# Kernel optimization log

Hardware: AMD Instinct MI355X
Metric: run time of the kernel (lower is better)

The kernel has to match this reference:

```python
import jax, jax.numpy as jnp
import numpy as np

F_FIELDS = 39
VOCAB = 100000
EMB = 16
BATCH = 16384
H1, H2 = 32, 32


def setup_inputs() -> dict:
    key = jax.random.key(0)
    ks = jax.random.split(key, 10)
    Xi = jax.random.randint(ks[0], (BATCH, F_FIELDS, 1), 0, VOCAB, dtype=jnp.int64 if jax.config.jax_enable_x64 else jnp.int32).astype(jnp.int32)
    Xv = jax.random.uniform(ks[1], (BATCH, F_FIELDS), dtype=jnp.float32)
    # per-field embedding tables, stacked (all feature_sizes equal)
    emb1 = jax.random.normal(ks[2], (F_FIELDS, VOCAB, 1), dtype=jnp.float32)
    emb2 = jax.random.normal(ks[3], (F_FIELDS, VOCAB, EMB), dtype=jnp.float32)
    d_in = F_FIELDS * EMB
    W1 = jax.random.normal(ks[4], (d_in, H1), dtype=jnp.float32) / np.sqrt(d_in)
    b1 = jnp.zeros((H1,), dtype=jnp.float32)
    W2 = jax.random.normal(ks[5], (H1, H2), dtype=jnp.float32) / np.sqrt(H1)
    b2 = jnp.zeros((H2,), dtype=jnp.float32)
    bias = jax.random.normal(ks[6], (1,), dtype=jnp.float32)
    return {"Xi": Xi, "Xv": Xv, "emb1": emb1, "emb2": emb2,
            "W1": W1, "b1": b1, "W2": W2, "b2": b2, "bias": bias}


def reference(Xi, Xv, emb1, emb2, W1, b1, W2, b2, bias):
    B = Xi.shape[0]
    idx = Xi[:, :, 0]  # [B, F]
    # flatten per-field tables into one big table; offset indices by field
    off = idx + (jnp.arange(F_FIELDS, dtype=idx.dtype) * VOCAB)[None, :]  # [B, F]
    # first order: gather scalar per (b, f), scale by Xv
    first = emb1.reshape(F_FIELDS * VOCAB)[off] * Xv  # [B, F]
    # second order embeddings, scaled by Xv
    e2 = emb2.reshape(F_FIELDS * VOCAB, EMB)[off] * Xv[:, :, None]  # [B, F, E]
    s = jnp.sum(e2, axis=1)                      # [B, E]
    sq_sum = jnp.sum(e2 * e2, axis=1)            # [B, E]
    fm_second = 0.5 * (s * s - sq_sum)           # [B, E]
    # deep part on concatenated field embeddings
    deep_in = e2.reshape(B, F_FIELDS * EMB)
    h = jax.nn.relu(deep_in @ W1 + b1)
    h = jax.nn.relu(h @ W2 + b2)
    total = jnp.sum(first, axis=1) + jnp.sum(fm_second, axis=1) + jnp.sum(h, axis=1) + bias
    return total  # [B]
```

## Files before the change

### kernel.cpp

```cpp
#include <hip/hip_runtime.h>
#include <hip/hip_bf16.h>

#define F_FIELDS 39
#define VOCAB    100000
#define EMB      16
#define BATCH    16384
#define H1       32
#define H2       32
#define KSTEPS   20
#define KPW      10

typedef __bf16 bf16x8 __attribute__((ext_vector_type(8)));
typedef float  f32x4  __attribute__((ext_vector_type(4)));

__global__ __launch_bounds__(256) void swizzle_w1_kernel(const float* __restrict__ W1,
                                                         __bf16* __restrict__ ws)
{
    int fidx = blockIdx.x * 256 + threadIdx.x;
    if (fidx >= KSTEPS * 2 * 64) return;
    int lane = fidx & 63;
    int nh   = (fidx >> 6) & 1;
    int ks   = fidx >> 7;
    int k0   = ks * 32 + (lane >> 4) * 8;
    int n    = nh * 16 + (lane & 15);
    __bf16 vals[8];
    #pragma unroll
    for (int j = 0; j < 8; ++j) {
        int k = k0 + j;
        vals[j] = (k < F_FIELDS * EMB) ? (__bf16)W1[k * H1 + n] : (__bf16)0.0f;
    }
    *reinterpret_cast<bf16x8*>(&ws[fidx * 8]) = *reinterpret_cast<const bf16x8*>(vals);
}

__global__ __launch_bounds__(128, 2) void deepfm_main(
    const int*   __restrict__ Xi,  const float* __restrict__ Xv,
    const float* __restrict__ emb1,const float* __restrict__ emb2,
    const __bf16* __restrict__ wsW1,
    const float* __restrict__ b1,  const float* __restrict__ W2,
    const float* __restrict__ b2,  const float* __restrict__ bias,
    float* __restrict__ out)
{
    __shared__ float pacc[2][16][32];
    __shared__ float sbuf[2][16][16];
    __shared__ float qbuf[2][16];
    __shared__ float fbuf[2][16];
    __shared__ float W2s[H1 * H2];

    const int t    = threadIdx.x;
    const int h    = t >> 6;
    const int l    = t & 63;
    const int sloc = l & 15;
    const int q    = l >> 4;
    const int fpar = q >> 1;
    const int eoff = (q & 1) * 8;
    const int sample = blockIdx.x * 16 + sloc;
    const int xbase  = sample * F_FIELDS;

    #pragma unroll
    for (int i = 0; i < 2; ++i)
        reinterpret_cast<float4*>(W2s)[t + 128 * i] =
            reinterpret_cast<const float4*>(W2)[t + 128 * i];

    int   idxm[KPW]; float xvm[KPW];
    #pragma unroll
    for (int ks = 0; ks < KPW; ++ks) {
        int f = 4 * ks + 2 * h + fpar;
        bool v = (f < F_FIELDS);
        int fi = v ? f : 0;
        idxm[ks] = Xi[xbase + fi];
        xvm[ks]  = v ? Xv[xbase + fi] : 0.0f;
    }
    int idxf[5]; float xvf[5];
    #pragma unroll
    for (int i = 0; i < 5; ++i) {
        int f = h * 4 + q + 8 * i;
        bool v = (f < F_FIELDS);
        int fi = v ? f : 0;
        idxf[i] = Xi[xbase + fi];
        xvf[i]  = v ? Xv[xbase + fi] : 0.0f;
    }

    float4 g0[KPW], g1[KPW];
    bf16x8 fr0[KPW], fr1[KPW];
    const bf16x8* wsf = reinterpret_cast<const bf16x8*>(wsW1);
    #pragma unroll
    for (int ks = 0; ks < KPW; ++ks) {
        int f = 4 * ks + 2 * h + fpar;
        int fi = (f < F_FIELDS) ? f : 0;
        int off = (fi * VOCAB + idxm[ks]) * EMB + eoff;
        const float4* rp = reinterpret_cast<const float4*>(emb2 + off);
        g0[ks] = rp[0];
        g1[ks] = rp[1];
        int kstep = 2 * ks + h;
        fr0[ks] = wsf[(kstep * 2 + 0) * 64 + l];
        fr1[ks] = wsf[(kstep * 2 + 1) * 64 + l];
    }
    float e1v[5];
    #pragma unroll
    for (int i = 0; i < 5; ++i) {
        int f = h * 4 + q + 8 * i;
        int fi = (f < F_FIELDS) ? f : 0;
        e1v[i] = emb1[fi * VOCAB + idxf[i]];
    }

    f32x4 acc0 = {0.f,0.f,0.f,0.f}, acc1 = {0.f,0.f,0.f,0.f};
    float sa[8], sq[8];
    #pragma unroll
    for (int j = 0; j < 8; ++j) { sa[j] = 0.f; sq[j] = 0.f; }

    #pragma unroll
    for (int ks = 0; ks < KPW; ++ks) {
        float xv = xvm[ks];
        float e[8] = { g0[ks].x*xv, g0[ks].y*xv, g0[ks].z*xv, g0[ks].w*xv,
                       g1[ks].x*xv, g1[ks].y*xv, g1[ks].z*xv, g1[ks].w*xv };
        bf16x8 a;
        #pragma unroll
        for (int j = 0; j < 8; ++j) {
            a[j] = (__bf16)e[j];
            sa[j] += e[j];
            sq[j] += e[j]*e[j];
        }
        acc0 = __builtin_amdgcn_mfma_f32_16x16x32_bf16(a, fr0[ks], acc0, 0, 0, 0);
        acc1 = __builtin_amdgcn_mfma_f32_16x16x32_bf16(a, fr1[ks], acc1, 0, 0, 0);
    }

    float sf[8];
    float qq = 0.f;
    #pragma unroll
    for (int j = 0; j < 8; ++j) {
        sf[j] = sa[j] + __shfl_xor(sa[j], 32);
        qq   += sq[j];
    }
    qq += __shfl_xor(qq, 32);
    qq += __shfl_xor(qq, 16);
    if (q < 2) {
        float4 v0 = make_float4(sf[0], sf[1], sf[2], sf[3]);
        float4 v1 = make_float4(sf[4], sf[5], sf[6], sf[7]);
        float4* srow = reinterpret_cast<float4*>(&sbuf[h][sloc][q * 8]);
        srow[0] = v0; srow[1] = v1;
    }
    if (l < 16) qbuf[h][sloc] = qq;

    float facc = 0.f;
    #pragma unroll
    for (int i = 0; i < 5; ++i) facc += e1v[i] * xvf[i];
    facc += __shfl_xor(facc, 16);
    facc += __shfl_xor(facc, 32);
    if (l < 16) fbuf[h][sloc] = facc;

    float badd0 = (h == 0) ? b1[sloc]      : 0.f;
    float badd1 = (h == 0) ? b1[16 + sloc] : 0.f;
    #pragma unroll
    for (int r = 0; r < 4; ++r) {
        int row = q * 4 + r;
        pacc[h][row][sloc]      = acc0[r] + badd0;
        pacc[h][row][16 + sloc] = acc1[r] + badd1;
    }
    __syncthreads();

    const int s = t >> 3;
    const int u = t & 7;

    float s2 = 0.f;
    #pragma unroll
    for (int p = 0; p < 2; ++p) {
        int pos = u * 2 + p;
        float sv = sbuf[0][s][pos] + sbuf[1][s][pos];
        s2 += sv * sv;
    }

    float a4[4];
    #pragma unroll
    for (int c = 0; c < 4; ++c) a4[c] = b2[u * 4 + c];
    #pragma unroll
    for (int i = 0; i < H1; ++i) {
        float hv = fmaxf(pacc[0][s][i] + pacc[1][s][i], 0.f);
        const float* wr = &W2s[i * H2 + u * 4];
        #pragma unroll
        for (int c = 0; c < 4; ++c) a4[c] += hv * wr[c];
    }
    float psum = 0.f;
    #pragma unroll
    for (int c = 0; c < 4; ++c) psum += fmaxf(a4[c], 0.f);

    psum += __shfl_xor(psum, 1);
    psum += __shfl_xor(psum, 2);
    psum += __shfl_xor(psum, 4);
    s2   += __shfl_xor(s2, 1);
    s2   += __shfl_xor(s2, 2);
    s2   += __shfl_xor(s2, 4);

    if (u == 0) {
        float qtot = qbuf[0][s] + qbuf[1][s];
        float ftot = fbuf[0][s] + fbuf[1][s];
        out[blockIdx.x * 16 + s] = psum + 0.5f * (s2 - qtot) + ftot + bias[0];
    }
}

extern "C" void kernel_launch(void* const* d_in, const int* in_sizes, int n_in,
                              void* d_out, int out_size, void* d_ws, size_t ws_size,
                              hipStream_t stream) {
    const int*   Xi   = (const int*)  d_in[0];
    const float* Xv   = (const float*)d_in[1];
    const float* emb1 = (const float*)d_in[2];
    const float* emb2 = (const float*)d_in[3];
    const float* W1   = (const float*)d_in[4];
    const float* b1   = (const float*)d_in[5];
    const float* W2   = (const float*)d_in[6];
    const float* b2   = (const float*)d_in[7];
    const float* bias = (const float*)d_in[8];
    float* out = (float*)d_out;
    __bf16* ws = (__bf16*)d_ws;

    swizzle_w1_kernel<<<(KSTEPS*2*64 + 255)/256, 256, 0, stream>>>(W1, ws);
    deepfm_main<<<BATCH/16, 128, 0, stream>>>(Xi, Xv, emb1, emb2, ws, b1, W2, b2, bias, out);
}
```

Baseline: 35.44 us.

## Split each 16-sample block across four waves and stage indices in LDS

Doubles the block to 256 threads so four waves share the K dimension of each 16-sample tile. Each wave now issues half as many embedding gathers, which lowers register pressure and raises occupancy. Xi and Xv are staged cooperatively through LDS with coalesced loads, and the W1 fragments are loaded inside the MFMA loop instead of all up front. The W2 layer is split so each thread computes two outputs after a shared hidden-activation buffer. This adds an extra __syncthreads and LDS traffic, and issues fewer outstanding loads per thread.

```diff
diff --git a/kernel.cpp b/kernel.cpp
--- a/kernel.cpp
+++ b/kernel.cpp
@@ -8,7 +8,7 @@
 #define H1       32
 #define H2       32
 #define KSTEPS   20
-#define KPW      10
+#define KPW      5
 
 typedef __bf16 bf16x8 __attribute__((ext_vector_type(8)));
 typedef float  f32x4  __attribute__((ext_vector_type(4)));
@@ -32,7 +32,7 @@
     *reinterpret_cast<bf16x8*>(&ws[fidx * 8]) = *reinterpret_cast<const bf16x8*>(vals);
 }
 
-__global__ __launch_bounds__(128, 2) void deepfm_main(
+__global__ __launch_bounds__(256, 4) void deepfm_main(
     const int*   __restrict__ Xi,  const float* __restrict__ Xv,
     const float* __restrict__ emb1,const float* __restrict__ emb2,
     const __bf16* __restrict__ wsW1,
@@ -40,11 +40,14 @@
     const float* __restrict__ b2,  const float* __restrict__ bias,
     float* __restrict__ out)
 {
-    __shared__ float pacc[2][16][32];
-    __shared__ float sbuf[2][16][16];
-    __shared__ float qbuf[2][16];
-    __shared__ float fbuf[2][16];
+    __shared__ int   sXi[16 * F_FIELDS];
+    __shared__ float sXv[16 * F_FIELDS];
+    __shared__ float pacc[4][16][32];
+    __shared__ float sbuf[4][16][16];
+    __shared__ float qbuf[4][16];
+    __shared__ float fbuf[4][16];
     __shared__ float W2s[H1 * H2];
+    __shared__ float hs[16][32];
 
     const int t    = threadIdx.x;
     const int h    = t >> 6;
@@ -53,63 +56,55 @@
     const int q    = l >> 4;
     const int fpar = q >> 1;
     const int eoff = (q & 1) * 8;
-    const int sample = blockIdx.x * 16 + sloc;
-    const int xbase  = sample * F_FIELDS;
-
-    #pragma unroll
-    for (int i = 0; i < 2; ++i)
-        reinterpret_cast<float4*>(W2s)[t + 128 * i] =
-            reinterpret_cast<const float4*>(W2)[t + 128 * i];
-
-    int   idxm[KPW]; float xvm[KPW];
+    const int blk  = blockIdx.x;
+
+    {
+        const int base = blk * 16 * F_FIELDS;
+        #pragma unroll
+        for (int i = t; i < 16 * F_FIELDS; i += 256) {
+            sXi[i] = Xi[base + i];
+            sXv[i] = Xv[base + i];
+        }
+    }
+    reinterpret_cast<float4*>(W2s)[t] = reinterpret_cast<const float4*>(W2)[t];
+    __syncthreads();
+
+    float xvm[KPW];
+    float4 g0[KPW], g1[KPW];
     #pragma unroll
     for (int ks = 0; ks < KPW; ++ks) {
-        int f = 4 * ks + 2 * h + fpar;
+        int f = 8 * ks + 2 * h + fpar;
         bool v = (f < F_FIELDS);
         int fi = v ? f : 0;
-        idxm[ks] = Xi[xbase + fi];
-        xvm[ks]  = v ? Xv[xbase + fi] : 0.0f;
-    }
-    int idxf[5]; float xvf[5];
-    #pragma unroll
-    for (int i = 0; i < 5; ++i) {
-        int f = h * 4 + q + 8 * i;
+        int idx = sXi[sloc * F_FIELDS + fi];
+        xvm[ks] = v ? sXv[sloc * F_FIELDS + fi] : 0.0f;
+        const float4* rp = reinterpret_cast<const float4*>(emb2 + (fi * VOCAB + idx) * EMB + eoff);
+        g0[ks] = rp[0];
+        g1[ks] = rp[1];
+    }
+    float e1v[3]; float xvf[3];
+    #pragma unroll
+    for (int i = 0; i < 3; ++i) {
+        int f = 4 * h + q + 16 * i;
         bool v = (f < F_FIELDS);
         int fi = v ? f : 0;
-        idxf[i] = Xi[xbase + fi];
-        xvf[i]  = v ? Xv[xbase + fi] : 0.0f;
-    }
-
-    float4 g0[KPW], g1[KPW];
-    bf16x8 fr0[KPW], fr1[KPW];
+        int idx = sXi[sloc * F_FIELDS + fi];
+        xvf[i] = v ? sXv[sloc * F_FIELDS + fi] : 0.0f;
+        e1v[i] = emb1[fi * VOCAB + idx];
+    }
+
     const bf16x8* wsf = reinterpret_cast<const bf16x8*>(wsW1);
+    f32x4 acc0 = {0.f,0.f,0.f,0.f}, acc1 = {0.f,0.f,0.f,0.f};
+    float sa[8];
+    float qq = 0.f;
+    #pragma unroll
+    for (int j = 0; j < 8; ++j) sa[j] = 0.f;
+
     #pragma unroll
     for (int ks = 0; ks < KPW; ++ks) {
-        int f = 4 * ks + 2 * h + fpar;
-        int fi = (f < F_FIELDS) ? f : 0;
-        int off = (fi * VOCAB + idxm[ks]) * EMB + eoff;
-        const float4* rp = reinterpret_cast<const float4*>(emb2 + off);
-        g0[ks] = rp[0];
-        g1[ks] = rp[1];
-        int kstep = 2 * ks + h;
-        fr0[ks] = wsf[(kstep * 2 + 0) * 64 + l];
-        fr1[ks] = wsf[(kstep * 2 + 1) * 64 + l];
-    }
-    float e1v[5];
-    #pragma unroll
-    for (int i = 0; i < 5; ++i) {
-        int f = h * 4 + q + 8 * i;
-        int fi = (f < F_FIELDS) ? f : 0;
-        e1v[i] = emb1[fi * VOCAB + idxf[i]];
-    }
-
-    f32x4 acc0 = {0.f,0.f,0.f,0.f}, acc1 = {0.f,0.f,0.f,0.f};
-    float sa[8], sq[8];
-    #pragma unroll
-    for (int j = 0; j < 8; ++j) { sa[j] = 0.f; sq[j] = 0.f; }
-
-    #pragma unroll
-    for (int ks = 0; ks < KPW; ++ks) {
+        int kstep = 4 * ks + h;
+        bf16x8 fr0 = wsf[(kstep * 2 + 0) * 64 + l];
+        bf16x8 fr1 = wsf[(kstep * 2 + 1) * 64 + l];
         float xv = xvm[ks];
         float e[8] = { g0[ks].x*xv, g0[ks].y*xv, g0[ks].z*xv, g0[ks].w*xv,
                        g1[ks].x*xv, g1[ks].y*xv, g1[ks].z*xv, g1[ks].w*xv };
@@ -118,32 +113,27 @@
         for (int j = 0; j < 8; ++j) {
             a[j] = (__bf16)e[j];
             sa[j] += e[j];
-            sq[j] += e[j]*e[j];
+            qq   += e[j]*e[j];
         }
-        acc0 = __builtin_amdgcn_mfma_f32_16x16x32_bf16(a, fr0[ks], acc0, 0, 0, 0);
-        acc1 = __builtin_amdgcn_mfma_f32_16x16x32_bf16(a, fr1[ks], acc1, 0, 0, 0);
+        acc0 = __builtin_amdgcn_mfma_f32_16x16x32_bf16(a, fr0, acc0, 0, 0, 0);
+        acc1 = __builtin_amdgcn_mfma_f32_16x16x32_bf16(a, fr1, acc1, 0, 0, 0);
     }
 
     float sf[8];
-    float qq = 0.f;
-    #pragma unroll
-    for (int j = 0; j < 8; ++j) {
-        sf[j] = sa[j] + __shfl_xor(sa[j], 32);
-        qq   += sq[j];
-    }
+    #pragma unroll
+    for (int j = 0; j < 8; ++j) sf[j] = sa[j] + __shfl_xor(sa[j], 32);
     qq += __shfl_xor(qq, 32);
     qq += __shfl_xor(qq, 16);
     if (q < 2) {
-        float4 v0 = make_float4(sf[0], sf[1], sf[2], sf[3]);
-        float4 v1 = make_float4(sf[4], sf[5], sf[6], sf[7]);
         float4* srow = reinterpret_cast<float4*>(&sbuf[h][sloc][q * 8]);
-        srow[0] = v0; srow[1] = v1;
+        srow[0] = make_float4(sf[0], sf[1], sf[2], sf[3]);
+        srow[1] = make_float4(sf[4], sf[5], sf[6], sf[7]);
     }
     if (l < 16) qbuf[h][sloc] = qq;
 
     float facc = 0.f;
     #pragma unroll
-    for (int i = 0; i < 5; ++i) facc += e1v[i] * xvf[i];
+    for (int i = 0; i < 3; ++i) facc += e1v[i] * xvf[i];
     facc += __shfl_xor(facc, 16);
     facc += __shfl_xor(facc, 32);
     if (l < 16) fbuf[h][sloc] = facc;
@@ -158,42 +148,37 @@
     }
     __syncthreads();
 
-    const int s = t >> 3;
-    const int u = t & 7;
-
-    float s2 = 0.f;
-    #pragma unroll
-    for (int p = 0; p < 2; ++p) {
-        int pos = u * 2 + p;
-        float sv = sbuf[0][s][pos] + sbuf[1][s][pos];
-        s2 += sv * sv;
-    }
-
-    float a4[4];
-    #pragma unroll
-    for (int c = 0; c < 4; ++c) a4[c] = b2[u * 4 + c];
+    {
+        int s = t >> 4, c = t & 15;
+        hs[s][c]      = fmaxf(pacc[0][s][c]      + pacc[1][s][c]      + pacc[2][s][c]      + pacc[3][s][c],      0.f);
+        hs[s][c + 16] = fmaxf(pacc[0][s][c + 16] + pacc[1][s][c + 16] + pacc[2][s][c + 16] + pacc[3][s][c + 16], 0.f);
+    }
+    __syncthreads();
+
+    const int s = t >> 4;
+    const int u = t & 15;
+
+    float sv = sbuf[0][s][u] + sbuf[1][s][u] + sbuf[2][s][u] + sbuf[3][s][u];
+    float s2 = sv * sv;
+
+    float a0 = b2[2 * u], a1 = b2[2 * u + 1];
     #pragma unroll
     for (int i = 0; i < H1; ++i) {
-        float hv = fmaxf(pacc[0][s][i] + pacc[1][s][i], 0.f);
-        const float* wr = &W2s[i * H2 + u * 4];
-        #pragma unroll
-        for (int c = 0; c < 4; ++c) a4[c] += hv * wr[c];
-    }
-    float psum = 0.f;
-    #pragma unroll
-    for (int c = 0; c < 4; ++c) psum += fmaxf(a4[c], 0.f);
-
-    psum += __shfl_xor(psum, 1);
-    psum += __shfl_xor(psum, 2);
-    psum += __shfl_xor(psum, 4);
-    s2   += __shfl_xor(s2, 1);
-    s2   += __shfl_xor(s2, 2);
-    s2   += __shfl_xor(s2, 4);
+        float hv = hs[s][i];
+        a0 += hv * W2s[i * H2 + 2 * u];
+        a1 += hv * W2s[i * H2 + 2 * u + 1];
+    }
+    float psum = fmaxf(a0, 0.f) + fmaxf(a1, 0.f);
+
+    psum += __shfl_xor(psum, 1);  s2 += __shfl_xor(s2, 1);
+    psum += __shfl_xor(psum, 2);  s2 += __shfl_xor(s2, 2);
+    psum += __shfl_xor(psum, 4);  s2 += __shfl_xor(s2, 4);
+    psum += __shfl_xor(psum, 8);  s2 += __shfl_xor(s2, 8);
 
     if (u == 0) {
-        float qtot = qbuf[0][s] + qbuf[1][s];
-        float ftot = fbuf[0][s] + fbuf[1][s];
-        out[blockIdx.x * 16 + s] = psum + 0.5f * (s2 - qtot) + ftot + bias[0];
+        float qtot = qbuf[0][s] + qbuf[1][s] + qbuf[2][s] + qbuf[3][s];
+        float ftot = fbuf[0][s] + fbuf[1][s] + fbuf[2][s] + fbuf[3][s];
+        out[blk * 16 + s] = psum + 0.5f * (s2 - qtot) + ftot + bias[0];
     }
 }
 
@@ -213,5 +198,5 @@
     __bf16* ws = (__bf16*)d_ws;
 
     swizzle_w1_kernel<<<(KSTEPS*2*64 + 255)/256, 256, 0, stream>>>(W1, ws);
-    deepfm_main<<<BATCH/16, 128, 0, stream>>>(Xi, Xv, emb1, emb2, ws, b1, W2, b2, bias, out);
+    deepfm_main<<<BATCH/16, 256, 0, stream>>>(Xi, Xv, emb1, emb2, ws, b1, W2, b2, bias, out);
 }
```

After: 34.62 us. 2.3% less time.
